# Optimization experiments

Hardware: AMD Instinct MI355X
Metric: run time of the kernel (lower is better)

## Reference

```python
import jax, jax.numpy as jnp
import numpy as np

B, S, H, D = 4, 2048, 16, 64


def setup_inputs() -> dict:
    key = jax.random.key(0)
    k1, k2, k3 = jax.random.split(key, 3)
    qk = jax.random.normal(k1, (B, S, 2, H, D), dtype=jnp.float32)
    v = jax.random.normal(k2, (B, S, H, D), dtype=jnp.float32)
    n = jax.random.normal(k3, (B, S, H), dtype=jnp.float32)
    return {"qk": qk, "v": v, "n": n}


def reference(qk, v, n):
    # qk: (B,S,2,H,D); v: (B,S,H,D); n: (B,S,H)
    q = qk[:, :, 0]  # (B,S,H,D)
    k = qk[:, :, 1]  # (B,S,H,D)
    seqlen = qk.shape[1]
    # causal raw scores: (B,H,T,S)
    scores = jnp.einsum('bthd,bshd->bhts', q, k)
    mask = jnp.tril(jnp.ones((seqlen, seqlen), dtype=scores.dtype))
    # exp normalizer per (b,h,t)
    n_bht = jnp.exp(jnp.transpose(n, (0, 2, 1)))  # (B,H,S)
    attention = scores * mask / n_bht[:, :, :, None]
    # output: (B,T,H,D)
    out = jnp.einsum('bhts,bshd->bthd', attention, v)
    return out
```

## Files before the change

### kernel.cpp

```cpp
#include <hip/hip_runtime.h>
#include <math.h>

#define B_ 4
#define S_ 2048
#define H_ 16
#define D_ 64
#define C_ 128
#define NC_ (S_ / C_)
#define BH_ (B_ * H_)
#define SPLIT_ 4

__global__ __launch_bounds__(256) void kv_chunk_kernel(
    const float* __restrict__ qk, const float* __restrict__ v,
    float* __restrict__ kvbuf)
{
  __shared__ float Kl[C_][D_];
  __shared__ float Vl[C_][D_];
  const int bid = blockIdx.x;
  const int bh = bid / NC_, c = bid % NC_;
  const int b = bh / H_, h = bh % H_;
  const int t0 = c * C_;
  const int tid = threadIdx.x;

  const size_t kbase = (((size_t)b * S_ * 2 + 1) * H_ + h) * D_;
  const size_t vbase = (((size_t)b * S_) * H_ + h) * D_;

  #pragma unroll
  for (int i = 0; i < 8; ++i) {
    int f = tid + i * 256;
    int row = f >> 4, c4 = (f & 15) << 2;
    size_t t = (size_t)t0 + row;
    *reinterpret_cast<float4*>(&Kl[row][c4]) =
        *reinterpret_cast<const float4*>(qk + kbase + t * (2 * H_ * D_) + c4);
    *reinterpret_cast<float4*>(&Vl[row][c4]) =
        *reinterpret_cast<const float4*>(v + vbase + t * (H_ * D_) + c4);
  }
  __syncthreads();

  const int dkt = tid >> 4;
  const int dvt = tid & 15;
  float acc[4][4] = {};
  #pragma unroll 4
  for (int s = 0; s < C_; ++s) {
    float4 k4 = *reinterpret_cast<const float4*>(&Kl[s][dkt * 4]);
    float4 v4 = *reinterpret_cast<const float4*>(&Vl[s][dvt * 4]);
    float kk[4] = {k4.x, k4.y, k4.z, k4.w};
    float vv[4] = {v4.x, v4.y, v4.z, v4.w};
    #pragma unroll
    for (int a = 0; a < 4; ++a)
      #pragma unroll
      for (int e = 0; e < 4; ++e)
        acc[a][e] += kk[a] * vv[e];
  }
  float* outp = kvbuf + (size_t)bid * (D_ * D_);
  #pragma unroll
  for (int a = 0; a < 4; ++a) {
    float4 o = make_float4(acc[a][0], acc[a][1], acc[a][2], acc[a][3]);
    *reinterpret_cast<float4*>(outp + (dkt * 4 + a) * D_ + dvt * 4) = o;
  }
}

__global__ __launch_bounds__(256) void prefix_kernel(float* __restrict__ kvbuf)
{
  const int bid = blockIdx.x;
  const int bh = bid / SPLIT_, part = bid % SPLIT_;
  const size_t off = (size_t)part * 1024 + (size_t)threadIdx.x * 4;
  float4 run = make_float4(0.f, 0.f, 0.f, 0.f);
  for (int c = 0; c < NC_; ++c) {
    float* p = kvbuf + ((size_t)bh * NC_ + c) * (D_ * D_) + off;
    float4 t = *reinterpret_cast<float4*>(p);
    *reinterpret_cast<float4*>(p) = run;
    run.x += t.x; run.y += t.y; run.z += t.z; run.w += t.w;
  }
}

__global__ __launch_bounds__(256) void out_kernel(
    const float* __restrict__ qk, const float* __restrict__ v,
    const float* __restrict__ nrm, const float* __restrict__ kvbuf,
    float* __restrict__ outp)
{
  __shared__ float Qt2[16][D_][8];
  __shared__ float Kt[D_][64];
  __shared__ float Sc[C_][64];

  const int bid = blockIdx.x;
  const int bh = bid / NC_, c = bid % NC_;
  const int b = bh / H_, h = bh % H_;
  const int t0 = c * C_;
  const int tid = threadIdx.x;
  const int TG = tid >> 4;
  const int SG = tid & 15;
  const int tb = TG * 8;
  const int key = TG & 7;

  {
    const int t = tid >> 1;
    const int d0 = (tid & 1) * 32;
    const int wtg = t >> 3, wrow = t & 7, wkey = wtg & 7;
    const float* qrow =
        qk + ((((size_t)b * S_ + t0 + t) * 2 + 0) * H_ + h) * D_ + d0;
    float tmp[32];
    #pragma unroll
    for (int i = 0; i < 8; ++i) {
      float4 x = *reinterpret_cast<const float4*>(qrow + i * 4);
      tmp[i*4+0] = x.x; tmp[i*4+1] = x.y; tmp[i*4+2] = x.z; tmp[i*4+3] = x.w;
    }
    #pragma unroll
    for (int i = 0; i < 32; ++i)
      Qt2[wtg][(d0 + i) ^ wkey][wrow] = tmp[i];
  }
  __syncthreads();

  float o[8][4] = {};

  if (c > 0) {
    const float* M = kvbuf + ((size_t)bh * NC_ + c) * (D_ * D_);
    #pragma unroll 4
    for (int dk = 0; dk < D_; ++dk) {
      const float* qp = &Qt2[TG][dk ^ key][0];
      float4 qa = *reinterpret_cast<const float4*>(qp);
      float4 qb = *reinterpret_cast<const float4*>(qp + 4);
      float4 m4 = *reinterpret_cast<const float4*>(M + dk * D_ + SG * 4);
      float qv[8] = {qa.x, qa.y, qa.z, qa.w, qb.x, qb.y, qb.z, qb.w};
      float mv[4] = {m4.x, m4.y, m4.z, m4.w};
      #pragma unroll
      for (int i = 0; i < 8; ++i)
        #pragma unroll
        for (int jj = 0; jj < 4; ++jj)
          o[i][jj] += qv[i] * mv[jj];
    }
  }

  const float* kbase2 = qk + ((((size_t)b * S_) * 2 + 1) * H_ + h) * D_;
  const float* vbase2 = v + (((size_t)b * S_) * H_ + h) * D_;

  for (int j = 0; j < 2; ++j) {
    if (j > 0) __syncthreads();
    {
      const int sl = tid >> 2;
      const int d0 = (tid & 3) * 16;
      const float* krow = kbase2 + (size_t)(t0 + j * 64 + sl) * (2 * H_ * D_) + d0;
      #pragma unroll
      for (int q4 = 0; q4 < 4; ++q4) {
        float4 kx = *reinterpret_cast<const float4*>(krow + q4 * 4);
        Kt[d0 + q4*4 + 0][sl] = kx.x;
        Kt[d0 + q4*4 + 1][sl] = kx.y;
        Kt[d0 + q4*4 + 2][sl] = kx.z;
        Kt[d0 + q4*4 + 3][sl] = kx.w;
      }
    }
    __syncthreads();

    const bool active = (tb >= j * 64);
    if (active) {
      float sc[8][4] = {};
      #pragma unroll 4
      for (int d = 0; d < D_; ++d) {
        const float* qp = &Qt2[TG][d ^ key][0];
        float4 qa = *reinterpret_cast<const float4*>(qp);
        float4 qb = *reinterpret_cast<const float4*>(qp + 4);
        float4 k4 = *reinterpret_cast<const float4*>(&Kt[d][SG * 4]);
        float qv[8] = {qa.x, qa.y, qa.z, qa.w, qb.x, qb.y, qb.z, qb.w};
        float kv[4] = {k4.x, k4.y, k4.z, k4.w};
        #pragma unroll
        for (int i = 0; i < 8; ++i)
          #pragma unroll
          for (int jj = 0; jj < 4; ++jj)
            sc[i][jj] += qv[i] * kv[jj];
      }
      #pragma unroll
      for (int i = 0; i < 8; ++i) {
        const int tl = tb + i;
        float4 w;
        w.x = (j*64 + SG*4 + 0 <= tl) ? sc[i][0] : 0.f;
        w.y = (j*64 + SG*4 + 1 <= tl) ? sc[i][1] : 0.f;
        w.z = (j*64 + SG*4 + 2 <= tl) ? sc[i][2] : 0.f;
        w.w = (j*64 + SG*4 + 3 <= tl) ? sc[i][3] : 0.f;
        *reinterpret_cast<float4*>(&Sc[tl][4 * (SG ^ key)]) = w;
      }
    }
    __syncthreads();

    if (active) {
      #pragma unroll 2
      for (int sq = 0; sq < 16; ++sq) {
        const int sg0 = t0 + j * 64 + sq * 4;
        float4 v0 = *reinterpret_cast<const float4*>(vbase2 + (size_t)(sg0+0) * (H_*D_) + SG*4);
        float4 v1 = *reinterpret_cast<const float4*>(vbase2 + (size_t)(sg0+1) * (H_*D_) + SG*4);
        float4 v2 = *reinterpret_cast<const float4*>(vbase2 + (size_t)(sg0+2) * (H_*D_) + SG*4);
        float4 v3 = *reinterpret_cast<const float4*>(vbase2 + (size_t)(sg0+3) * (H_*D_) + SG*4);
        const int scol = 4 * (sq ^ key);
        #pragma unroll
        for (int i = 0; i < 8; ++i) {
          float4 s4 = *reinterpret_cast<const float4*>(&Sc[tb + i][scol]);
          o[i][0] += s4.x*v0.x + s4.y*v1.x + s4.z*v2.x + s4.w*v3.x;
          o[i][1] += s4.x*v0.y + s4.y*v1.y + s4.z*v2.y + s4.w*v3.y;
          o[i][2] += s4.x*v0.z + s4.y*v1.z + s4.z*v2.z + s4.w*v3.z;
          o[i][3] += s4.x*v0.w + s4.y*v1.w + s4.z*v2.w + s4.w*v3.w;
        }
      }
    }
  }

  #pragma unroll
  for (int i = 0; i < 8; ++i) {
    const size_t t = (size_t)t0 + tb + i;
    float nv = nrm[((size_t)b * S_ + t) * H_ + h];
    float inv = expf(-nv);
    float4 ov = make_float4(o[i][0]*inv, o[i][1]*inv, o[i][2]*inv, o[i][3]*inv);
    *reinterpret_cast<float4*>(
        outp + (((size_t)b * S_ + t) * H_ + h) * D_ + SG * 4) = ov;
  }
}

extern "C" void kernel_launch(void* const* d_in, const int* in_sizes, int n_in,
                              void* d_out, int out_size, void* d_ws, size_t ws_size,
                              hipStream_t stream) {
  const float* qk  = (const float*)d_in[0];
  const float* v   = (const float*)d_in[1];
  const float* nrm = (const float*)d_in[2];
  float* out = (float*)d_out;
  float* kvbuf = (float*)d_ws;

  kv_chunk_kernel<<<dim3(BH_ * NC_), dim3(256), 0, stream>>>(qk, v, kvbuf);
  prefix_kernel<<<dim3(BH_ * SPLIT_), dim3(256), 0, stream>>>(kvbuf);
  out_kernel<<<dim3(BH_ * NC_), dim3(256), 0, stream>>>(qk, v, nrm, kvbuf, out);
}
```

Measured before the change: 207.9 us.

## Fuse chunk KV and prefix into a two-level scan; rebalance causal output threads

Replaces the per-chunk KV kernel and the separate prefix kernel with one scan kernel. Each block accumulates four chunks and writes exclusive local prefixes plus a group total. The output kernel then sums the needed group totals on the fly. The output kernel also moves to 512 threads, and each thread-group now owns two early and two late rows, so causal work is spread evenly instead of leaving half the threads idle in the second sub-block. This removes one launch and a pass over the kvbuf. In exchange it adds extra global reads of group totals inside the dk loop and makes the scan kernel serial over four chunks, with fewer blocks.

```diff
diff --git a/kernel.cpp b/kernel.cpp
--- a/kernel.cpp
+++ b/kernel.cpp
@@ -6,210 +6,212 @@
 #define H_ 16
 #define D_ 64
 #define C_ 128
-#define NC_ (S_ / C_)
-#define BH_ (B_ * H_)
-#define SPLIT_ 4
-
-__global__ __launch_bounds__(256) void kv_chunk_kernel(
+#define NC_ 16
+#define BH_ 64
+
+__global__ __launch_bounds__(256) void scan4_kernel(
     const float* __restrict__ qk, const float* __restrict__ v,
     float* __restrict__ kvbuf)
 {
   __shared__ float Kl[C_][D_];
   __shared__ float Vl[C_][D_];
   const int bid = blockIdx.x;
-  const int bh = bid / NC_, c = bid % NC_;
-  const int b = bh / H_, h = bh % H_;
-  const int t0 = c * C_;
+  const int bh = bid >> 2, cg = bid & 3;
+  const int b = bh >> 4, h = bh & 15;
   const int tid = threadIdx.x;
+  const int dkt = tid >> 4, dvt = tid & 15;
 
   const size_t kbase = (((size_t)b * S_ * 2 + 1) * H_ + h) * D_;
-  const size_t vbase = (((size_t)b * S_) * H_ + h) * D_;
-
+  const size_t vbase = ((size_t)b * S_ * H_ + h) * D_;
+
+  float run[4][4] = {};
+
+  for (int i = 0; i < 4; ++i) {
+    const int c = cg * 4 + i;
+    const int t0 = c * C_;
+    __syncthreads();
+    #pragma unroll
+    for (int u = 0; u < 8; ++u) {
+      int f = tid + u * 256;
+      int row = f >> 4, c4 = (f & 15) << 2;
+      size_t t = (size_t)t0 + row;
+      *reinterpret_cast<float4*>(&Kl[row][c4]) =
+          *reinterpret_cast<const float4*>(qk + kbase + t * (2*H_*D_) + c4);
+      *reinterpret_cast<float4*>(&Vl[row][c4]) =
+          *reinterpret_cast<const float4*>(v + vbase + t * (H_*D_) + c4);
+    }
+    if (i > 0) {
+      float* op = kvbuf + ((size_t)bh * NC_ + c) * (D_*D_);
+      #pragma unroll
+      for (int a = 0; a < 4; ++a)
+        *reinterpret_cast<float4*>(op + (dkt*4+a)*D_ + dvt*4) =
+            make_float4(run[a][0], run[a][1], run[a][2], run[a][3]);
+    }
+    __syncthreads();
+    #pragma unroll 4
+    for (int s = 0; s < C_; ++s) {
+      float4 k4 = *reinterpret_cast<const float4*>(&Kl[s][dkt*4]);
+      float4 v4 = *reinterpret_cast<const float4*>(&Vl[s][dvt*4]);
+      float kk[4] = {k4.x, k4.y, k4.z, k4.w};
+      float vv[4] = {v4.x, v4.y, v4.z, v4.w};
+      #pragma unroll
+      for (int a = 0; a < 4; ++a)
+        #pragma unroll
+        for (int e = 0; e < 4; ++e)
+          run[a][e] += kk[a] * vv[e];
+    }
+  }
+  float* tp = kvbuf + ((size_t)bh * NC_ + cg * 4) * (D_*D_);
   #pragma unroll
-  for (int i = 0; i < 8; ++i) {
-    int f = tid + i * 256;
-    int row = f >> 4, c4 = (f & 15) << 2;
-    size_t t = (size_t)t0 + row;
-    *reinterpret_cast<float4*>(&Kl[row][c4]) =
-        *reinterpret_cast<const float4*>(qk + kbase + t * (2 * H_ * D_) + c4);
-    *reinterpret_cast<float4*>(&Vl[row][c4]) =
-        *reinterpret_cast<const float4*>(v + vbase + t * (H_ * D_) + c4);
-  }
-  __syncthreads();
-
-  const int dkt = tid >> 4;
-  const int dvt = tid & 15;
-  float acc[4][4] = {};
-  #pragma unroll 4
-  for (int s = 0; s < C_; ++s) {
-    float4 k4 = *reinterpret_cast<const float4*>(&Kl[s][dkt * 4]);
-    float4 v4 = *reinterpret_cast<const float4*>(&Vl[s][dvt * 4]);
-    float kk[4] = {k4.x, k4.y, k4.z, k4.w};
-    float vv[4] = {v4.x, v4.y, v4.z, v4.w};
-    #pragma unroll
-    for (int a = 0; a < 4; ++a)
-      #pragma unroll
-      for (int e = 0; e < 4; ++e)
-        acc[a][e] += kk[a] * vv[e];
-  }
-  float* outp = kvbuf + (size_t)bid * (D_ * D_);
-  #pragma unroll
-  for (int a = 0; a < 4; ++a) {
-    float4 o = make_float4(acc[a][0], acc[a][1], acc[a][2], acc[a][3]);
-    *reinterpret_cast<float4*>(outp + (dkt * 4 + a) * D_ + dvt * 4) = o;
-  }
+  for (int a = 0; a < 4; ++a)
+    *reinterpret_cast<float4*>(tp + (dkt*4+a)*D_ + dvt*4) =
+        make_float4(run[a][0], run[a][1], run[a][2], run[a][3]);
 }
 
-__global__ __launch_bounds__(256) void prefix_kernel(float* __restrict__ kvbuf)
-{
-  const int bid = blockIdx.x;
-  const int bh = bid / SPLIT_, part = bid % SPLIT_;
-  const size_t off = (size_t)part * 1024 + (size_t)threadIdx.x * 4;
-  float4 run = make_float4(0.f, 0.f, 0.f, 0.f);
-  for (int c = 0; c < NC_; ++c) {
-    float* p = kvbuf + ((size_t)bh * NC_ + c) * (D_ * D_) + off;
-    float4 t = *reinterpret_cast<float4*>(p);
-    *reinterpret_cast<float4*>(p) = run;
-    run.x += t.x; run.y += t.y; run.z += t.z; run.w += t.w;
-  }
-}
-
-__global__ __launch_bounds__(256) void out_kernel(
+__global__ __launch_bounds__(512, 4) void out_kernel(
     const float* __restrict__ qk, const float* __restrict__ v,
     const float* __restrict__ nrm, const float* __restrict__ kvbuf,
     float* __restrict__ outp)
 {
-  __shared__ float Qt2[16][D_][8];
+  __shared__ float Qt2[32][D_][4];
   __shared__ float Kt[D_][64];
   __shared__ float Sc[C_][64];
 
   const int bid = blockIdx.x;
   const int bh = bid / NC_, c = bid % NC_;
-  const int b = bh / H_, h = bh % H_;
+  const int b = bh >> 4, h = bh & 15;
   const int t0 = c * C_;
   const int tid = threadIdx.x;
-  const int TG = tid >> 4;
-  const int SG = tid & 15;
-  const int tb = TG * 8;
+  const int TG = tid >> 4, SG = tid & 15;
   const int key = TG & 7;
 
   {
-    const int t = tid >> 1;
-    const int d0 = (tid & 1) * 32;
-    const int wtg = t >> 3, wrow = t & 7, wkey = wtg & 7;
+    const int row = tid >> 2;
+    const int d0 = (tid & 3) * 16;
+    const int otg  = (row < 64) ? (row >> 1) : ((row - 64) >> 1);
+    const int slot = (row < 64) ? (row & 1) : (2 + (row & 1));
+    const int okey = otg & 7;
     const float* qrow =
-        qk + ((((size_t)b * S_ + t0 + t) * 2 + 0) * H_ + h) * D_ + d0;
-    float tmp[32];
-    #pragma unroll
-    for (int i = 0; i < 8; ++i) {
-      float4 x = *reinterpret_cast<const float4*>(qrow + i * 4);
-      tmp[i*4+0] = x.x; tmp[i*4+1] = x.y; tmp[i*4+2] = x.z; tmp[i*4+3] = x.w;
-    }
-    #pragma unroll
-    for (int i = 0; i < 32; ++i)
-      Qt2[wtg][(d0 + i) ^ wkey][wrow] = tmp[i];
+        qk + ((((size_t)(b * S_ + t0 + row)) * 2 + 0) * H_ + h) * D_ + d0;
+    float tmp[16];
+    #pragma unroll
+    for (int u = 0; u < 4; ++u) {
+      float4 x = *reinterpret_cast<const float4*>(qrow + u * 4);
+      tmp[u*4+0] = x.x; tmp[u*4+1] = x.y; tmp[u*4+2] = x.z; tmp[u*4+3] = x.w;
+    }
+    #pragma unroll
+    for (int u = 0; u < 16; ++u)
+      Qt2[otg][(d0 + u) ^ okey][slot] = tmp[u];
   }
   __syncthreads();
 
-  float o[8][4] = {};
+  float o[4][4] = {};
 
   if (c > 0) {
-    const float* M = kvbuf + ((size_t)bh * NC_ + c) * (D_ * D_);
+    const int ng = c >> 2;
+    const bool has_local = (c & 3) != 0;
+    const float* M0 = kvbuf + ((size_t)bh * NC_ + c) * (D_*D_);
+    const float* T0 = kvbuf + ((size_t)bh * NC_) * (D_*D_);
     #pragma unroll 4
     for (int dk = 0; dk < D_; ++dk) {
-      const float* qp = &Qt2[TG][dk ^ key][0];
-      float4 qa = *reinterpret_cast<const float4*>(qp);
-      float4 qb = *reinterpret_cast<const float4*>(qp + 4);
-      float4 m4 = *reinterpret_cast<const float4*>(M + dk * D_ + SG * 4);
-      float qv[8] = {qa.x, qa.y, qa.z, qa.w, qb.x, qb.y, qb.z, qb.w};
+      float4 m4 = make_float4(0.f, 0.f, 0.f, 0.f);
+      if (has_local)
+        m4 = *reinterpret_cast<const float4*>(M0 + dk * D_ + SG * 4);
+      for (int g = 0; g < ng; ++g) {
+        float4 t4 = *reinterpret_cast<const float4*>(
+            T0 + (size_t)(4 * g) * (D_*D_) + dk * D_ + SG * 4);
+        m4.x += t4.x; m4.y += t4.y; m4.z += t4.z; m4.w += t4.w;
+      }
+      float4 qq = *reinterpret_cast<const float4*>(&Qt2[TG][dk ^ key][0]);
+      float qv[4] = {qq.x, qq.y, qq.z, qq.w};
       float mv[4] = {m4.x, m4.y, m4.z, m4.w};
       #pragma unroll
-      for (int i = 0; i < 8; ++i)
+      for (int sl = 0; sl < 4; ++sl)
         #pragma unroll
         for (int jj = 0; jj < 4; ++jj)
-          o[i][jj] += qv[i] * mv[jj];
-    }
-  }
-
-  const float* kbase2 = qk + ((((size_t)b * S_) * 2 + 1) * H_ + h) * D_;
-  const float* vbase2 = v + (((size_t)b * S_) * H_ + h) * D_;
-
+          o[sl][jj] += qv[sl] * mv[jj];
+    }
+  }
+
+  const float* kbase2 = qk + (((size_t)b * S_ * 2 + 1) * H_ + h) * D_;
+  const float* vbase2 = v + ((size_t)b * S_ * H_ + h) * D_;
+  const int rown[4] = {TG*2, TG*2+1, 64+TG*2, 65+TG*2};
+
+  #pragma unroll
   for (int j = 0; j < 2; ++j) {
-    if (j > 0) __syncthreads();
+    const int sbase = j * 64;
+    __syncthreads();
     {
-      const int sl = tid >> 2;
-      const int d0 = (tid & 3) * 16;
-      const float* krow = kbase2 + (size_t)(t0 + j * 64 + sl) * (2 * H_ * D_) + d0;
-      #pragma unroll
-      for (int q4 = 0; q4 < 4; ++q4) {
-        float4 kx = *reinterpret_cast<const float4*>(krow + q4 * 4);
-        Kt[d0 + q4*4 + 0][sl] = kx.x;
-        Kt[d0 + q4*4 + 1][sl] = kx.y;
-        Kt[d0 + q4*4 + 2][sl] = kx.z;
-        Kt[d0 + q4*4 + 3][sl] = kx.w;
+      const int sl = tid & 63;
+      const int d0 = (tid >> 6) * 8;
+      const float* krow = kbase2 + (size_t)(t0 + sbase + sl) * (2*H_*D_) + d0;
+      float4 ka = *reinterpret_cast<const float4*>(krow);
+      float4 kb = *reinterpret_cast<const float4*>(krow + 4);
+      Kt[d0+0][sl] = ka.x; Kt[d0+1][sl] = ka.y;
+      Kt[d0+2][sl] = ka.z; Kt[d0+3][sl] = ka.w;
+      Kt[d0+4][sl] = kb.x; Kt[d0+5][sl] = kb.y;
+      Kt[d0+6][sl] = kb.z; Kt[d0+7][sl] = kb.w;
+    }
+    __syncthreads();
+
+    const int slo = (j == 0) ? 0 : 2;
+    float sc[4][4] = {};
+    #pragma unroll 4
+    for (int d = 0; d < D_; ++d) {
+      float4 qq = *reinterpret_cast<const float4*>(&Qt2[TG][d ^ key][0]);
+      float4 k4 = *reinterpret_cast<const float4*>(&Kt[d][SG * 4]);
+      float qv[4] = {qq.x, qq.y, qq.z, qq.w};
+      float kv[4] = {k4.x, k4.y, k4.z, k4.w};
+      #pragma unroll
+      for (int sl = 0; sl < 4; ++sl) {
+        if (sl < slo) continue;
+        #pragma unroll
+        for (int jj = 0; jj < 4; ++jj)
+          sc[sl][jj] += qv[sl] * kv[jj];
       }
     }
-    __syncthreads();
-
-    const bool active = (tb >= j * 64);
-    if (active) {
-      float sc[8][4] = {};
-      #pragma unroll 4
-      for (int d = 0; d < D_; ++d) {
-        const float* qp = &Qt2[TG][d ^ key][0];
-        float4 qa = *reinterpret_cast<const float4*>(qp);
-        float4 qb = *reinterpret_cast<const float4*>(qp + 4);
-        float4 k4 = *reinterpret_cast<const float4*>(&Kt[d][SG * 4]);
-        float qv[8] = {qa.x, qa.y, qa.z, qa.w, qb.x, qb.y, qb.z, qb.w};
-        float kv[4] = {k4.x, k4.y, k4.z, k4.w};
-        #pragma unroll
-        for (int i = 0; i < 8; ++i)
-          #pragma unroll
-          for (int jj = 0; jj < 4; ++jj)
-            sc[i][jj] += qv[i] * kv[jj];
+    #pragma unroll
+    for (int sl = 0; sl < 4; ++sl) {
+      if (sl < slo) continue;
+      const int r = rown[sl];
+      float4 w;
+      w.x = (sbase + SG*4 + 0 <= r) ? sc[sl][0] : 0.f;
+      w.y = (sbase + SG*4 + 1 <= r) ? sc[sl][1] : 0.f;
+      w.z = (sbase + SG*4 + 2 <= r) ? sc[sl][2] : 0.f;
+      w.w = (sbase + SG*4 + 3 <= r) ? sc[sl][3] : 0.f;
+      *reinterpret_cast<float4*>(&Sc[r][4 * (SG ^ key)]) = w;
+    }
+    __syncthreads();
+
+    #pragma unroll 2
+    for (int sq = 0; sq < 16; ++sq) {
+      const size_t sg0 = (size_t)t0 + sbase + sq * 4;
+      float4 v0 = *reinterpret_cast<const float4*>(vbase2 + (sg0+0)*(H_*D_) + SG*4);
+      float4 v1 = *reinterpret_cast<const float4*>(vbase2 + (sg0+1)*(H_*D_) + SG*4);
+      float4 v2 = *reinterpret_cast<const float4*>(vbase2 + (sg0+2)*(H_*D_) + SG*4);
+      float4 v3 = *reinterpret_cast<const float4*>(vbase2 + (sg0+3)*(H_*D_) + SG*4);
+      const int scol = 4 * (sq ^ key);
+      #pragma unroll
+      for (int sl = 0; sl < 4; ++sl) {
+        if (sl < slo) continue;
+        float4 s4 = *reinterpret_cast<const float4*>(&Sc[rown[sl]][scol]);
+        o[sl][0] += s4.x*v0.x + s4.y*v1.x + s4.z*v2.x + s4.w*v3.x;
+        o[sl][1] += s4.x*v0.y + s4.y*v1.y + s4.z*v2.y + s4.w*v3.y;
+        o[sl][2] += s4.x*v0.z + s4.y*v1.z + s4.z*v2.z + s4.w*v3.z;
+        o[sl][3] += s4.x*v0.w + s4.y*v1.w + s4.z*v2.w + s4.w*v3.w;
       }
-      #pragma unroll
-      for (int i = 0; i < 8; ++i) {
-        const int tl = tb + i;
-        float4 w;
-        w.x = (j*64 + SG*4 + 0 <= tl) ? sc[i][0] : 0.f;
-        w.y = (j*64 + SG*4 + 1 <= tl) ? sc[i][1] : 0.f;
-        w.z = (j*64 + SG*4 + 2 <= tl) ? sc[i][2] : 0.f;
-        w.w = (j*64 + SG*4 + 3 <= tl) ? sc[i][3] : 0.f;
-        *reinterpret_cast<float4*>(&Sc[tl][4 * (SG ^ key)]) = w;
-      }
-    }
-    __syncthreads();
-
-    if (active) {
-      #pragma unroll 2
-      for (int sq = 0; sq < 16; ++sq) {
-        const int sg0 = t0 + j * 64 + sq * 4;
-        float4 v0 = *reinterpret_cast<const float4*>(vbase2 + (size_t)(sg0+0) * (H_*D_) + SG*4);
-        float4 v1 = *reinterpret_cast<const float4*>(vbase2 + (size_t)(sg0+1) * (H_*D_) + SG*4);
-        float4 v2 = *reinterpret_cast<const float4*>(vbase2 + (size_t)(sg0+2) * (H_*D_) + SG*4);
-        float4 v3 = *reinterpret_cast<const float4*>(vbase2 + (size_t)(sg0+3) * (H_*D_) + SG*4);
-        const int scol = 4 * (sq ^ key);
-        #pragma unroll
-        for (int i = 0; i < 8; ++i) {
-          float4 s4 = *reinterpret_cast<const float4*>(&Sc[tb + i][scol]);
-          o[i][0] += s4.x*v0.x + s4.y*v1.x + s4.z*v2.x + s4.w*v3.x;
-          o[i][1] += s4.x*v0.y + s4.y*v1.y + s4.z*v2.y + s4.w*v3.y;
-          o[i][2] += s4.x*v0.z + s4.y*v1.z + s4.z*v2.z + s4.w*v3.z;
-          o[i][3] += s4.x*v0.w + s4.y*v1.w + s4.z*v2.w + s4.w*v3.w;
-        }
-      }
     }
   }
 
   #pragma unroll
-  for (int i = 0; i < 8; ++i) {
-    const size_t t = (size_t)t0 + tb + i;
-    float nv = nrm[((size_t)b * S_ + t) * H_ + h];
+  for (int sl = 0; sl < 4; ++sl) {
+    const size_t t = (size_t)t0 + rown[sl];
+    float nv = nrm[((size_t)(b * S_) + t) * H_ + h];
     float inv = expf(-nv);
-    float4 ov = make_float4(o[i][0]*inv, o[i][1]*inv, o[i][2]*inv, o[i][3]*inv);
+    float4 ov = make_float4(o[sl][0]*inv, o[sl][1]*inv,
+                            o[sl][2]*inv, o[sl][3]*inv);
     *reinterpret_cast<float4*>(
-        outp + (((size_t)b * S_ + t) * H_ + h) * D_ + SG * 4) = ov;
+        outp + (((size_t)(b * S_) + t) * H_ + h) * D_ + SG * 4) = ov;
   }
 }
 
@@ -222,7 +224,6 @@
   float* out = (float*)d_out;
   float* kvbuf = (float*)d_ws;
 
-  kv_chunk_kernel<<<dim3(BH_ * NC_), dim3(256), 0, stream>>>(qk, v, kvbuf);
-  prefix_kernel<<<dim3(BH_ * SPLIT_), dim3(256), 0, stream>>>(kvbuf);
-  out_kernel<<<dim3(BH_ * NC_), dim3(256), 0, stream>>>(qk, v, nrm, kvbuf, out);
+  scan4_kernel<<<dim3(BH_ * 4), dim3(256), 0, stream>>>(qk, v, kvbuf);
+  out_kernel<<<dim3(BH_ * NC_), dim3(512), 0, stream>>>(qk, v, nrm, kvbuf, out);
 }
```

Measured after the change: 304.1 us. 1.46x slower.
